# Kernel optimization log

Measured on AMD Instinct MI355X. Metric: run time of the kernel, lower is better.

The kernel has to match this reference:

```python
import jax, jax.numpy as jnp
import numpy as np

B, CIN, COUT, K, N = 4, 64, 64, 16, 32768


def setup_inputs() -> dict:
    key = jax.random.key(0)
    k1, k2, k3, k4, k5 = jax.random.split(key, 5)
    features = jax.random.normal(k1, (B, CIN, N), dtype=jnp.float32)
    neighborhood = jax.random.randint(k2, (B, K, N), 0, N, dtype=jnp.int32)
    positions = jax.random.normal(k3, (B, 3, N), dtype=jnp.float32)
    # kaiming-uniform-style init for params
    bt = float(np.sqrt(6.0 / (CIN * COUT)))
    weight_theta = jax.random.uniform(k4, (3, CIN, COUT), jnp.float32, -bt, bt)
    bb = float(np.sqrt(6.0 / CIN))
    weight_bias = jax.random.uniform(k5, (CIN, COUT), jnp.float32, -bb, bb)
    bias = jnp.zeros((COUT,), dtype=jnp.float32)
    return {"features": features, "weight_theta": weight_theta,
            "weight_bias": weight_bias, "bias": bias,
            "neighborhood": neighborhood, "positions": positions}


def reference(features, weight_theta, weight_bias, bias, neighborhood, positions):
    # features: [B, Cin, N]; neighborhood: [B, K, N]; positions: [B, 3, N]
    gather = jax.vmap(lambda f, nb: f[:, nb])  # [C, N], [K, N] -> [C, K, N]
    f_g = gather(features, neighborhood)           # [B, Cin, K, N]
    p_g = gather(positions, neighborhood)          # [B, 3, K, N]
    dp = p_g - positions[:, :, None, :]            # relative positions [B, 3, K, N]
    # position-dependent linear term: contract over neighbors first
    S = jnp.einsum('bckn,bdkn->bdcn', f_g, dp)     # [B, 3, Cin, N]
    fsum = f_g.sum(axis=2)                         # [B, Cin, N]
    out = (jnp.einsum('bdcn,dco->bon', S, weight_theta)
           + jnp.einsum('bcn,co->bon', fsum, weight_bias))  # [B, Cout, N]
    return out + bias[None, :, None]
```

## Files before the change

### kernel.cpp

```cpp
#include <hip/hip_runtime.h>

#define B_    4
#define CIN   64
#define COUT  64
#define KN    16
#define NPTS  32768
#define NPB   32

typedef __fp16 f16;
typedef __attribute__((ext_vector_type(8))) __fp16 half8;
typedef __attribute__((ext_vector_type(2))) __fp16 half2v;
typedef __attribute__((ext_vector_type(4))) float  f32x4;

static __device__ __forceinline__ half2v uint_as_h2(unsigned u) {
  union { unsigned u; half2v h; } c; c.u = u; return c.h;
}
static __device__ __forceinline__ unsigned h2_as_uint(half2v h) {
  union { unsigned u; half2v h; } c; c.h = h; return c.u;
}

static __device__ __forceinline__ float dot2_acc(half2v a, half2v b, float acc) {
#if __has_builtin(__builtin_amdgcn_fdot2)
  return __builtin_amdgcn_fdot2(a, b, acc, false);
#else
  return acc + (float)a.x * (float)b.x + (float)a.y * (float)b.y;
#endif
}

__global__ __launch_bounds__(256) void prep_all_kernel(
    const float* __restrict__ f,
    const float* __restrict__ pos,
    const int*   __restrict__ nb,
    const float* __restrict__ wtheta,
    const float* __restrict__ wbias,
    f16*         __restrict__ ft,
    unsigned*    __restrict__ recG,
    f16*         __restrict__ Wt)
{
  __shared__ union {
    float    tile[64][65];
    unsigned recs[64][33];
  } sm;

  const int b    = blockIdx.y;
  const int n0   = blockIdx.x * 64;
  const int lane = threadIdx.x & 63;
  const int g    = threadIdx.x >> 6;

  const float* src = f + (size_t)b * CIN * NPTS + n0;
#pragma unroll
  for (int cc = 0; cc < 16; ++cc)
    sm.tile[cc * 4 + g][lane] = src[(size_t)(cc * 4 + g) * NPTS + lane];
  __syncthreads();
  f16* dst = ft + ((size_t)b * NPTS + n0) * CIN;
  const int nrow = threadIdx.x >> 5;
  const int c2   = (threadIdx.x & 31) * 2;
#pragma unroll
  for (int pass = 0; pass < 8; ++pass) {
    const int n = pass * 8 + nrow;
    half2v v = __builtin_amdgcn_cvt_pkrtz(sm.tile[c2][n], sm.tile[c2 + 1][n]);
    *(half2v*)&dst[(size_t)n * CIN + c2] = v;
  }
  __syncthreads();

  {
    const int p  = threadIdx.x & 63;
    const int kh = threadIdx.x >> 6;
    const int n  = n0 + p;
    const float* pb = pos + (size_t)b * 3 * NPTS;
    const float cx = pb[n], cy = pb[NPTS + n], cz = pb[2 * NPTS + n];
    const int* nbb = nb + (size_t)b * KN * NPTS + n;
    int idx[4]; float dx[4], dy[4], dz[4];
#pragma unroll
    for (int j = 0; j < 4; ++j) {
      const int k = kh * 4 + j;
      idx[j] = nbb[(size_t)k * NPTS];
      dx[j] = pb[idx[j]] - cx;
      dy[j] = pb[NPTS + idx[j]] - cy;
      dz[j] = pb[2 * NPTS + idx[j]] - cz;
    }
#pragma unroll
    for (int jj = 0; jj < 2; ++jj) {
      const int dw = kh * 2 + jj;
      sm.recs[p][dw] = (unsigned)idx[2 * jj] | ((unsigned)idx[2 * jj + 1] << 16);
      sm.recs[p][8  + dw] = h2_as_uint(__builtin_amdgcn_cvt_pkrtz(dx[2 * jj], dx[2 * jj + 1]));
      sm.recs[p][16 + dw] = h2_as_uint(__builtin_amdgcn_cvt_pkrtz(dy[2 * jj], dy[2 * jj + 1]));
      sm.recs[p][24 + dw] = h2_as_uint(__builtin_amdgcn_cvt_pkrtz(dz[2 * jj], dz[2 * jj + 1]));
    }
  }

  if (b == 0 && blockIdx.x < 64) {
    const int t  = blockIdx.x * 256 + threadIdx.x;
    const int o  = t >> 8;
    const int cp = t & 255;
    const int c  = cp >> 2;
    const int d  = cp & 3;
    const float v = (d < 3) ? wtheta[((size_t)d * 64 + c) * 64 + o]
                            : wbias[(size_t)c * 64 + o];
    Wt[t] = (f16)v;
  }
  __syncthreads();

  {
    const int p = threadIdx.x >> 2;
    const int q = threadIdx.x & 3;
    unsigned* gdst = recG + ((size_t)b * NPTS + n0) * 32 + (size_t)threadIdx.x * 8;
#pragma unroll
    for (int j = 0; j < 8; ++j) gdst[j] = sm.recs[p][q * 8 + j];
  }
}

__global__ __launch_bounds__(256) void flex_fused_kernel(
    const unsigned short* __restrict__ ftu,
    const unsigned* __restrict__ recG,
    const f16*      __restrict__ Wt,
    const float*    __restrict__ bias,
    float*          __restrict__ out)
{
  __shared__ f16 TL[NPB][272];

  const int t    = threadIdx.x;
  const int lane = t & 63;
  const int wv   = __builtin_amdgcn_readfirstlane(t >> 6);

  const int xcd = blockIdx.x & 7;
  const int b   = xcd >> 1;
  const int loc = (xcd & 1) * ((NPTS / NPB) >> 1) + (blockIdx.x >> 3);
  const int n0  = loc * NPB;

  const char* fpk = (const char*)(ftu + (size_t)b * NPTS * CIN);
  const unsigned* recp = recG + ((size_t)b * NPTS + n0 + wv * 8) * 32;
  const half2v one2 = {(__fp16)1.0f, (__fp16)1.0f};

#pragma unroll
  for (int p = 0; p < 8; ++p) {
    const unsigned* rp = recp + p * 32;
    unsigned iw[8];
#pragma unroll
    for (int j = 0; j < 8; ++j) iw[j] = rp[j];
    unsigned fvv[16];
#pragma unroll
    for (int k = 0; k < 16; ++k) {
      const unsigned off =
          (((k & 1) ? (iw[k >> 1] >> 16) : (iw[k >> 1] & 0xffffu)) << 7);
      fvv[k] = *(const unsigned short*)(fpk + off + lane * 2);
    }
    float s0 = 0.f, s1 = 0.f, s2 = 0.f, fs = 0.f;
#pragma unroll
    for (int kk = 0; kk < 8; ++kk) {
      const half2v fp = uint_as_h2(fvv[2 * kk] | (fvv[2 * kk + 1] << 16));
      s0 = dot2_acc(uint_as_h2(rp[8  + kk]), fp, s0);
      s1 = dot2_acc(uint_as_h2(rp[16 + kk]), fp, s1);
      s2 = dot2_acc(uint_as_h2(rp[24 + kk]), fp, s2);
      fs = dot2_acc(one2, fp, fs);
    }
    uint2 pk;
    pk.x = h2_as_uint(__builtin_amdgcn_cvt_pkrtz(s0, s1));
    pk.y = h2_as_uint(__builtin_amdgcn_cvt_pkrtz(s2, fs));
    *(uint2*)&TL[wv * 8 + p][lane * 4] = pk;
  }
  __syncthreads();

  {
    const int col  = lane & 15;
    const int krow = lane >> 4;
    const f16* wr = Wt + (size_t)(wv * 16 + col) * 256 + krow * 8;
    half8 a[8];
#pragma unroll
    for (int kk = 0; kk < 8; ++kk) a[kk] = *(const half8*)(wr + kk * 32);

    f32x4 acc[2];
    acc[0] = (f32x4){0.f, 0.f, 0.f, 0.f};
    acc[1] = (f32x4){0.f, 0.f, 0.f, 0.f};
#pragma unroll
    for (int nt = 0; nt < 2; ++nt) {
      const f16* tc = &TL[nt * 16 + col][0] + krow * 8;
#pragma unroll
      for (int kk = 0; kk < 8; ++kk) {
        half8 bf = *(const half8*)(tc + kk * 32);
        acc[nt] = __builtin_amdgcn_mfma_f32_16x16x32_f16(a[kk], bf, acc[nt], 0, 0, 0);
      }
    }

    const float4 bv = *(const float4*)(bias + wv * 16 + krow * 4);
    float* ob = out + ((size_t)b * COUT + wv * 16 + krow * 4) * NPTS + n0 + col;
#pragma unroll
    for (int r = 0; r < 4; ++r) {
      const float badd = (r == 0) ? bv.x : (r == 1) ? bv.y : (r == 2) ? bv.z : bv.w;
      float* orow = ob + (size_t)r * NPTS;
#pragma unroll
      for (int nt = 0; nt < 2; ++nt)
        __builtin_nontemporal_store(acc[nt][r] + badd, orow + nt * 16);
    }
  }
}

extern "C" void kernel_launch(void* const* d_in, const int* in_sizes, int n_in,
                              void* d_out, int out_size, void* d_ws, size_t ws_size,
                              hipStream_t stream) {
  const float* features = (const float*)d_in[0];
  const float* wtheta   = (const float*)d_in[1];
  const float* wbias    = (const float*)d_in[2];
  const float* bias     = (const float*)d_in[3];
  const int*   nb       = (const int*)  d_in[4];
  const float* pos      = (const float*)d_in[5];
  float* out = (float*)d_out;

  char* ws = (char*)d_ws;
  f16*      ft  = (f16*)ws;
  f16*      Wt  = (f16*)(ws + 16777216);
  unsigned* rec = (unsigned*)(ws + 16777216 + 32768);

  prep_all_kernel<<<dim3(NPTS / 64, B_), 256, 0, stream>>>(
      features, pos, nb, wtheta, wbias, ft, rec, Wt);
  flex_fused_kernel<<<B_ * (NPTS / NPB), 256, 0, stream>>>(
      (const unsigned short*)ft, rec, Wt, bias, out);
}
```

Before: 153.0 us.

## Pack positions into float4 AoS and cap unroll/occupancy in fused kernel

Adds a kernel that repacks the SoA positions into a float4 array per point, so each neighbor gather in the prep kernel fetches one 16-byte load instead of three scattered 4-byte loads. The fused kernel gets a launch-bounds occupancy hint of 4 and partial unrolling of the point loop to cut register pressure. This costs an extra launch plus an extra pass over the positions buffer, and the reduced unroll may expose gather latency.

Result: faster. 141.4 us (-7.5%).

```diff
diff --git a/kernel.cpp b/kernel.cpp
--- a/kernel.cpp
+++ b/kernel.cpp
@@ -18,7 +18,6 @@
 static __device__ __forceinline__ unsigned h2_as_uint(half2v h) {
   union { unsigned u; half2v h; } c; c.h = h; return c.u;
 }
-
 static __device__ __forceinline__ float dot2_acc(half2v a, half2v b, float acc) {
 #if __has_builtin(__builtin_amdgcn_fdot2)
   return __builtin_amdgcn_fdot2(a, b, acc, false);
@@ -27,15 +26,28 @@
 #endif
 }
 
+__global__ __launch_bounds__(256) void pos_pack_kernel(
+    const float* __restrict__ p, float4* __restrict__ pt) {
+  const int b = blockIdx.y;
+  const int n = blockIdx.x * 256 + threadIdx.x;
+  const float* src = p + (size_t)b * 3 * NPTS;
+  float4 v;
+  v.x = src[n];
+  v.y = src[NPTS + n];
+  v.z = src[2 * NPTS + n];
+  v.w = 0.f;
+  pt[(size_t)b * NPTS + n] = v;
+}
+
 __global__ __launch_bounds__(256) void prep_all_kernel(
-    const float* __restrict__ f,
-    const float* __restrict__ pos,
-    const int*   __restrict__ nb,
-    const float* __restrict__ wtheta,
-    const float* __restrict__ wbias,
-    f16*         __restrict__ ft,
-    unsigned*    __restrict__ recG,
-    f16*         __restrict__ Wt)
+    const float*  __restrict__ f,
+    const float4* __restrict__ pt,
+    const int*    __restrict__ nb,
+    const float*  __restrict__ wtheta,
+    const float*  __restrict__ wbias,
+    f16*          __restrict__ ft,
+    unsigned*     __restrict__ recG,
+    f16*          __restrict__ Wt)
 {
   __shared__ union {
     float    tile[64][65];
@@ -67,17 +79,18 @@
     const int p  = threadIdx.x & 63;
     const int kh = threadIdx.x >> 6;
     const int n  = n0 + p;
-    const float* pb = pos + (size_t)b * 3 * NPTS;
-    const float cx = pb[n], cy = pb[NPTS + n], cz = pb[2 * NPTS + n];
+    const float4* ptb = pt + (size_t)b * NPTS;
+    const float4  ctr = ptb[n];
     const int* nbb = nb + (size_t)b * KN * NPTS + n;
     int idx[4]; float dx[4], dy[4], dz[4];
 #pragma unroll
     for (int j = 0; j < 4; ++j) {
       const int k = kh * 4 + j;
       idx[j] = nbb[(size_t)k * NPTS];
-      dx[j] = pb[idx[j]] - cx;
-      dy[j] = pb[NPTS + idx[j]] - cy;
-      dz[j] = pb[2 * NPTS + idx[j]] - cz;
+      const float4 q = ptb[idx[j]];
+      dx[j] = q.x - ctr.x;
+      dy[j] = q.y - ctr.y;
+      dz[j] = q.z - ctr.z;
     }
 #pragma unroll
     for (int jj = 0; jj < 2; ++jj) {
@@ -110,7 +123,7 @@
   }
 }
 
-__global__ __launch_bounds__(256) void flex_fused_kernel(
+__global__ __launch_bounds__(256, 4) void flex_fused_kernel(
     const unsigned short* __restrict__ ftu,
     const unsigned* __restrict__ recG,
     const f16*      __restrict__ Wt,
@@ -132,7 +145,7 @@
   const unsigned* recp = recG + ((size_t)b * NPTS + n0 + wv * 8) * 32;
   const half2v one2 = {(__fp16)1.0f, (__fp16)1.0f};
 
-#pragma unroll
+#pragma unroll 2
   for (int p = 0; p < 8; ++p) {
     const unsigned* rp = recp + p * 32;
     unsigned iw[8];
@@ -208,11 +221,13 @@
 
   char* ws = (char*)d_ws;
   f16*      ft  = (f16*)ws;
-  f16*      Wt  = (f16*)(ws + 16777216);
-  unsigned* rec = (unsigned*)(ws + 16777216 + 32768);
-
+  float4*   pt  = (float4*)(ws + 16777216);
+  f16*      Wt  = (f16*)(ws + 16777216 + 2097152);
+  unsigned* rec = (unsigned*)(ws + 16777216 + 2097152 + 32768);
+
+  pos_pack_kernel<<<dim3(NPTS / 256, B_), 256, 0, stream>>>(pos, pt);
   prep_all_kernel<<<dim3(NPTS / 64, B_), 256, 0, stream>>>(
-      features, pos, nb, wtheta, wbias, ft, rec, Wt);
+      features, pt, nb, wtheta, wbias, ft, rec, Wt);
   flex_fused_kernel<<<B_ * (NPTS / NPB), 256, 0, stream>>>(
       (const unsigned short*)ft, rec, Wt, bias, out);
 }
```
